# Kernel tuning notes

Hardware: AMD Instinct MI355X
Metric: run time of the kernel (lower is better)

## Reference

```python
import jax, jax.numpy as jnp
import numpy as np

COEF_DIM = 256  # must match init_kwargs coef_dim


def setup_inputs() -> dict:
    key = jax.random.key(0)
    k1, k2 = jax.random.split(key)
    # times in [0,1); with curr_t=1, t_scaled = 2*t - 1 lies in [-1,1)
    t = jax.random.uniform(k1, (4, 131072), dtype=jnp.float32)
    # learned HiPPO coefficients (buffer `coef` in the torch module)
    coef = jax.random.normal(k2, (COEF_DIM,), dtype=jnp.float32)
    return {"t": t, "coef": coef, "curr_t": 1}


def reference(t, coef, curr_t):
    """Signal reconstruction: sum_{i=1..N} coef[i-1]*sqrt(2i+1)*P_i(2t/curr_t-1).

    Instead of N independent legendre_polynomial_p calls (O(N^2) work),
    run the three-term Legendre recurrence once with lax.scan, fusing the
    coef-weighted accumulation into the carry (O(N) work per time point).
    """
    x = 2.0 * t / curr_t - 1.0            # scaled times, same shape as t
    n = coef.shape[0]
    i = jnp.arange(1, n + 1, dtype=jnp.float32)
    w = coef * jnp.sqrt(2.0 * i + 1.0)    # per-degree weight, degree i=1..N

    def step(carry, wi):
        pm1, p, acc = carry               # P_{deg-1}, P_deg, running sum
        w_next, deg = wi                  # weight for degree deg+1
        # P_{deg+1} = ((2*deg+1)*x*P_deg - deg*P_{deg-1}) / (deg+1)
        p_next = ((2.0 * deg + 1.0) * x * p - deg * pm1) / (deg + 1.0)
        return (p, p_next, acc + w_next * p_next), None

    # P_0 = 1, P_1 = x; accumulator starts with the degree-1 term w[0]*P_1
    init = (jnp.ones_like(x), x, w[0] * x)
    degs = jnp.arange(1, n, dtype=jnp.float32)
    (_, _, out), _ = jax.lax.scan(step, init, (w[1:], degs))
    return out
```

## Files before the change

kernel.cpp:

```cpp
#include <hip/hip_runtime.h>


constexpr double csqrt(double v) {
    double r = v > 1.0 ? v : 1.0;
    for (int i = 0; i < 64; ++i) r = 0.5 * (r + v / r);
    return r;
}

template <int I>
struct Step {
    static __device__ __forceinline__ void run(const float x, float& qm1,
                                               float& q, float& acc,
                                               const float* __restrict__ coef) {
        constexpr float A = (float)((2.0 * I + 1.0) * csqrt(2.0 * I + 3.0) /
                                    ((I + 1.0) * csqrt(2.0 * I + 1.0)));
        constexpr float B = (float)((double)I * csqrt(2.0 * I + 3.0) /
                                    ((I + 1.0) * csqrt(2.0 * I - 1.0)));
        float u  = A * q;
        float v  = B * qm1;
        float qn = fmaf(x, u, -v);
        acc = fmaf(coef[I], qn, acc);
        qm1 = q;
        q   = qn;
        Step<I + 1>::run(x, qm1, q, acc, coef);
    }
};
template <>
struct Step<256> {
    static __device__ __forceinline__ void run(float, float&, float&, float&,
                                               const float*) {}
};

__global__ __launch_bounds__(256, 8) void hippo_kernel(
    const float* __restrict__ t,
    const float* __restrict__ coef,
    const int* __restrict__ curr_t,
    float* __restrict__ out,
    int n)
{
    const int gid = blockIdx.x * 256 + threadIdx.x;
    if (gid >= n) return;

    const float s = 2.0f / (float)curr_t[0];
    const float x = fmaf(t[gid], s, -1.0f);

    float qm1 = 1.0f;
    float q   = 1.7320508075688772f * x;
    float acc = coef[0] * q;

    Step<1>::run(x, qm1, q, acc, coef);

    out[gid] = acc;
}

extern "C" void kernel_launch(void* const* d_in, const int* in_sizes, int n_in,
                              void* d_out, int out_size, void* d_ws, size_t ws_size,
                              hipStream_t stream)
{
    const float* t      = (const float*)d_in[0];
    const float* coef   = (const float*)d_in[1];
    const int*   curr_t = (const int*)d_in[2];
    float*       out    = (float*)d_out;

    int n = in_sizes[0];
    int blocks = (n + 255) / 256;
    hippo_kernel<<<blocks, 256, 0, stream>>>(t, coef, curr_t, out, n);
}
```

Before: 65.42 us.

## Convert Legendre series to Chebyshev basis and evaluate with Clenshaw recurrence

```diff
diff --git a/kernel.cpp b/kernel.cpp
--- a/kernel.cpp
+++ b/kernel.cpp
@@ -1,40 +1,45 @@
 #include <hip/hip_runtime.h>
+#include <math.h>
 
 
-constexpr double csqrt(double v) {
-    double r = v > 1.0 ? v : 1.0;
-    for (int i = 0; i < 64; ++i) r = 0.5 * (r + v / r);
-    return r;
+#define NDEG 256
+
+__global__ __launch_bounds__(256) void leg2cheb(
+    const float* __restrict__ coef, float* __restrict__ c)
+{
+    __shared__ float lam[NDEG + 1];
+    __shared__ float wp[NDEG + 1];
+    __shared__ float scan[256];
+    const int tid = threadIdx.x;
+
+    scan[tid] = (tid == 0) ? 1.0f : (((float)tid - 0.5f) / (float)tid);
+    __syncthreads();
+    for (int off = 1; off < 256; off <<= 1) {
+        float v = (tid >= off) ? scan[tid - off] : 1.0f;
+        __syncthreads();
+        scan[tid] *= v;
+        __syncthreads();
+    }
+    const float SQRTPI = 1.7724538509055160f;
+    lam[tid] = SQRTPI * scan[tid];
+    if (tid == 255) lam[256] = lam[255] * (255.5f / 256.0f);
+    wp[tid + 1] = coef[tid] * sqrtf(2.0f * (float)(tid + 1) + 1.0f);
+    __syncthreads();
+
+    const int m = tid;
+    const float TWOOPI = 0.63661977236758134f;
+    float s = 0.0f;
+    for (int n = (m == 0 ? 2 : m); n <= NDEG; n += 2)
+        s += wp[n] * lam[(n - m) >> 1] * lam[(n + m) >> 1];
+    c[m] = s * TWOOPI * ((m == 0) ? 0.5f : 1.0f);
+    if (tid == 0)
+        c[NDEG] = wp[NDEG] * TWOOPI * lam[0] * lam[NDEG];
 }
 
-template <int I>
-struct Step {
-    static __device__ __forceinline__ void run(const float x, float& qm1,
-                                               float& q, float& acc,
-                                               const float* __restrict__ coef) {
-        constexpr float A = (float)((2.0 * I + 1.0) * csqrt(2.0 * I + 3.0) /
-                                    ((I + 1.0) * csqrt(2.0 * I + 1.0)));
-        constexpr float B = (float)((double)I * csqrt(2.0 * I + 3.0) /
-                                    ((I + 1.0) * csqrt(2.0 * I - 1.0)));
-        float u  = A * q;
-        float v  = B * qm1;
-        float qn = fmaf(x, u, -v);
-        acc = fmaf(coef[I], qn, acc);
-        qm1 = q;
-        q   = qn;
-        Step<I + 1>::run(x, qm1, q, acc, coef);
-    }
-};
-template <>
-struct Step<256> {
-    static __device__ __forceinline__ void run(float, float&, float&, float&,
-                                               const float*) {}
-};
-
-__global__ __launch_bounds__(256, 8) void hippo_kernel(
+__global__ __launch_bounds__(256, 8) void cheb_eval(
     const float* __restrict__ t,
-    const float* __restrict__ coef,
     const int* __restrict__ curr_t,
+    const float* __restrict__ c,
     float* __restrict__ out,
     int n)
 {
@@ -43,14 +48,16 @@
 
     const float s = 2.0f / (float)curr_t[0];
     const float x = fmaf(t[gid], s, -1.0f);
+    const float U = 2.0f * x;
 
-    float qm1 = 1.0f;
-    float q   = 1.7320508075688772f * x;
-    float acc = coef[0] * q;
-
-    Step<1>::run(x, qm1, q, acc, coef);
-
-    out[gid] = acc;
+    float b1 = 0.0f, b2 = 0.0f;
+#pragma unroll
+    for (int k = NDEG; k >= 1; --k) {
+        float bn = fmaf(U, b1, -b2) + c[k];
+        b2 = b1;
+        b1 = bn;
+    }
+    out[gid] = fmaf(x, b1, -b2) + c[0];
 }
 
 extern "C" void kernel_launch(void* const* d_in, const int* in_sizes, int n_in,
@@ -61,8 +68,10 @@
     const float* coef   = (const float*)d_in[1];
     const int*   curr_t = (const int*)d_in[2];
     float*       out    = (float*)d_out;
+    float*       c      = (float*)d_ws;
 
     int n = in_sizes[0];
+    leg2cheb<<<1, 256, 0, stream>>>(coef, c);
     int blocks = (n + 255) / 256;
-    hippo_kernel<<<blocks, 256, 0, stream>>>(t, coef, curr_t, out, n);
+    cheb_eval<<<blocks, 256, 0, stream>>>(t, curr_t, c, out, n);
 }
```

Result: slower. 71.31 us (+9.0%).

## Replace Legendre forward recurrence with Clenshaw backward summation on rescaled basis

Applied to the files above, without the earlier changes.

```diff
diff --git a/kernel.cpp b/kernel.cpp
--- a/kernel.cpp
+++ b/kernel.cpp
@@ -1,34 +1,54 @@
 #include <hip/hip_runtime.h>
+#include <math.h>
 
 
-constexpr double csqrt(double v) {
-    double r = v > 1.0 ? v : 1.0;
-    for (int i = 0; i < 64; ++i) r = 0.5 * (r + v / r);
-    return r;
+#define NDEG 256
+
+__device__ __forceinline__ float g_of(int i) {
+    const float fi = (float)i;
+    float r = 2.0f * rsqrtf(3.14159265358979f * fi);
+    float inv = 1.0f / fi;
+    float corr = 1.0f + inv * (-0.125f + inv * (0.0078125f + inv * 0.0048828125f));
+    float g = r * corr;
+    g = (i == 1) ? 1.0f          : g;
+    g = (i == 2) ? 0.75f         : g;
+    g = (i == 3) ? 0.625f        : g;
+    g = (i == 4) ? 0.546875f     : g;
+    g = (i == 5) ? 0.4921875f    : g;
+    g = (i == 6) ? 0.451171875f  : g;
+    g = (i == 7) ? 0.4189453125f : g;
+    return g;
 }
 
-template <int I>
-struct Step {
-    static __device__ __forceinline__ void run(const float x, float& qm1,
-                                               float& q, float& acc,
-                                               const float* __restrict__ coef) {
-        constexpr float A = (float)((2.0 * I + 1.0) * csqrt(2.0 * I + 3.0) /
-                                    ((I + 1.0) * csqrt(2.0 * I + 1.0)));
-        constexpr float B = (float)((double)I * csqrt(2.0 * I + 3.0) /
-                                    ((I + 1.0) * csqrt(2.0 * I - 1.0)));
-        float u  = A * q;
-        float v  = B * qm1;
-        float qn = fmaf(x, u, -v);
-        acc = fmaf(coef[I], qn, acc);
-        qm1 = q;
-        q   = qn;
-        Step<I + 1>::run(x, qm1, q, acc, coef);
+template <int K>
+__device__ __forceinline__ void step(const float U, float& b1, float& b2,
+                                     const float w) {
+    constexpr double d = (double)(K + 1);
+    constexpr float NB = (float)(-(4.0 * d * d) / (4.0 * d * d - 1.0));
+    float tt = fmaf(NB, b2, w);
+    float bn = fmaf(U, b1, tt);
+    b2 = b1;
+    b1 = bn;
+}
+
+template <int J>
+struct Chunk {
+    static __device__ __forceinline__ void run(const float U, float& b1,
+                                               float& b2,
+                                               const float4* __restrict__ w4,
+                                               float4 c, float4 cn) {
+        float4 c2 = w4[(J >= 2) ? (J - 2) : 0];
+        step<4 * J + 4>(U, b1, b2, c.w);
+        step<4 * J + 3>(U, b1, b2, c.z);
+        step<4 * J + 2>(U, b1, b2, c.y);
+        step<4 * J + 1>(U, b1, b2, c.x);
+        Chunk<J - 1>::run(U, b1, b2, w4, cn, c2);
     }
 };
 template <>
-struct Step<256> {
-    static __device__ __forceinline__ void run(float, float&, float&, float&,
-                                               const float*) {}
+struct Chunk<-1> {
+    static __device__ __forceinline__ void run(float, float&, float&,
+                                               const float4*, float4, float4) {}
 };
 
 __global__ __launch_bounds__(256, 8) void hippo_kernel(
@@ -38,19 +58,27 @@
     float* __restrict__ out,
     int n)
 {
-    const int gid = blockIdx.x * 256 + threadIdx.x;
+    __shared__ float4 w4[NDEG / 4];
+    float* wf = (float*)w4;
+
+    const int tid = threadIdx.x;
+    {
+        const int k = tid + 1;
+        wf[tid] = coef[tid] * sqrtf(2.0f * (float)k + 1.0f) * g_of(k);
+    }
+    __syncthreads();
+
+    const int gid = blockIdx.x * 256 + tid;
     if (gid >= n) return;
 
     const float s = 2.0f / (float)curr_t[0];
     const float x = fmaf(t[gid], s, -1.0f);
+    const float U = 2.0f * x;
 
-    float qm1 = 1.0f;
-    float q   = 1.7320508075688772f * x;
-    float acc = coef[0] * q;
+    float b1 = 0.0f, b2 = 0.0f;
+    Chunk<63>::run(U, b1, b2, w4, w4[63], w4[62]);
 
-    Step<1>::run(x, qm1, q, acc, coef);
-
-    out[gid] = acc;
+    out[gid] = fmaf(x, b1, -0.66666666666667f * b2);
 }
 
 extern "C" void kernel_launch(void* const* d_in, const int* in_sizes, int n_in,
```

New measurement: 64.24 us. No clear change (-1.8%).
